# Performance work log

Measured on AMD Instinct MI355X. Metric: run time of the kernel, lower is better.

## Reference

```python
import jax, jax.numpy as jnp
from jax import lax
import numpy as np

# dims
B, L, M = 16, 512, 32
PRED, P, S, D = 96, 16, 8, 128
NST, DC, EXP, NL = 16, 4, 2, 4
N = (L - P) // S + 1          # 63 patches
DI = EXP * D                  # 256 d_inner
DTR = (D + 15) // 16          # 8 dt_rank


def setup_inputs() -> dict:
    key = jax.random.key(0)
    ks = jax.random.split(key, 16)
    r = lambda i, shape, s=0.02: jax.random.normal(ks[i], shape, dtype=jnp.float32) * s
    return {
        "x": jax.random.normal(ks[0], (B, L, M), dtype=jnp.float32),
        "patch_w": r(1, (D, P), 0.1), "patch_b": jnp.zeros((D,), jnp.float32),
        "pos_embed": r(2, (1, N, D)),
        "alpha": jnp.ones((NL, NL), jnp.float32), "beta": jnp.ones((NL, NL), jnp.float32),
        "theta": jnp.ones((NL, NL + 1), jnp.float32), "gamma": jnp.ones((NL, NL), jnp.float32),
        "tok_norm_w": jnp.ones((NL, D), jnp.float32), "tok_norm_b": jnp.zeros((NL, D), jnp.float32),
        "ch_norm_w": jnp.ones((NL, D), jnp.float32), "ch_norm_b": jnp.zeros((NL, D), jnp.float32),
        # 3 Mamba roles per layer: 0=token, 1=channel-fwd, 2=channel-bwd
        "in_proj_w": r(3, (NL, 3, 2 * DI, D), 0.05),
        "conv_w": r(4, (NL, 3, DI, DC), 0.1), "conv_b": jnp.zeros((NL, 3, DI), jnp.float32),
        "x_proj_w": r(5, (NL, 3, DTR + 2 * NST, DI), 0.05),
        "dt_proj_w": r(6, (NL, 3, DI, DTR), 0.1), "dt_proj_b": r(7, (NL, 3, DI), 0.5),
        "A_log": jnp.broadcast_to(jnp.log(jnp.arange(1, NST + 1, dtype=jnp.float32)), (NL, 3, DI, NST)) + 0.0,
        "D_ssm": jnp.ones((NL, 3, DI), jnp.float32),
        "out_proj_w": r(8, (NL, 3, D, DI), 0.05),
        "n2d_w1": jnp.ones((D,), jnp.float32), "n2d_b1": jnp.zeros((D,), jnp.float32),
        "n2d_w2": jnp.ones((N,), jnp.float32), "n2d_b2": jnp.zeros((N,), jnp.float32),
        "head_w": r(9, (PRED, N * D), 0.01), "head_b": jnp.zeros((PRED,), jnp.float32),
    }


def _ln(x, w, b):
    mu = x.mean(-1, keepdims=True)
    var = x.var(-1, keepdims=True)
    return (x - mu) * lax.rsqrt(var + 1e-5) * w + b


def _mamba(x, in_w, cw, cb, xw, dtw, dtb, a_log, dp, out_w):
    """Standard Mamba block. x: (b, s, D) -> (b, s, D)."""
    bsz = x.shape[0]
    xz = x @ in_w.T                                   # (b,s,2*DI)
    xi, z = jnp.split(xz, 2, axis=-1)
    # causal depthwise conv over seq
    xt = jnp.pad(xi.transpose(0, 2, 1), ((0, 0), (0, 0), (DC - 1, 0)))
    conv = lax.conv_general_dilated(xt, cw[:, None, :], (1,), 'VALID',
                                    dimension_numbers=('NCH', 'OIH', 'NCH'),
                                    feature_group_count=DI)
    u = jax.nn.silu(conv + cb[None, :, None]).transpose(0, 2, 1)  # (b,s,DI)
    xdbl = u @ xw.T
    dt, Bm, Cm = jnp.split(xdbl, [DTR, DTR + NST], axis=-1)
    dt = jax.nn.softplus(dt @ dtw.T + dtb)            # (b,s,DI)
    A = -jnp.exp(a_log)                               # (DI,NST)

    def step(h, inp):
        dt_t, b_t, c_t, u_t = inp                     # (b,DI),(b,NST),(b,NST),(b,DI)
        h = h * jnp.exp(dt_t[:, :, None] * A) + (dt_t * u_t)[:, :, None] * b_t[:, None, :]
        return h, jnp.einsum('bdn,bn->bd', h, c_t)

    h0 = jnp.zeros((bsz, DI, NST), x.dtype)
    _, ys = lax.scan(step, h0, (dt.swapaxes(0, 1), Bm.swapaxes(0, 1),
                                Cm.swapaxes(0, 1), u.swapaxes(0, 1)))
    y = ys.swapaxes(0, 1) + u * dp                    # D skip
    y = y * jax.nn.silu(z)
    return y @ out_w.T


def reference(x, patch_w, patch_b, pos_embed, alpha, beta, theta, gamma,
              tok_norm_w, tok_norm_b, ch_norm_w, ch_norm_b,
              in_proj_w, conv_w, conv_b, x_proj_w, dt_proj_w, dt_proj_b,
              A_log, D_ssm, out_proj_w, n2d_w1, n2d_b1, n2d_w2, n2d_b2,
              head_w, head_b):
    means = x.mean(1, keepdims=True)
    stds = jnp.std(x, axis=1, keepdims=True, ddof=1) + 1e-5   # torch unbiased std
    xn = ((x - means) / stds).transpose(0, 2, 1)              # (B,M,L)
    idx = jnp.arange(N)[:, None] * S + jnp.arange(P)[None, :]
    patches = xn[:, :, idx].reshape(B * M, N, P)              # unfold
    h = patches @ patch_w.T + patch_b + pos_embed             # (B*M,N,D)

    def mp(l, r):
        return (in_proj_w[l, r], conv_w[l, r], conv_b[l, r], x_proj_w[l, r],
                dt_proj_w[l, r], dt_proj_b[l, r], A_log[l, r], D_ssm[l, r], out_proj_w[l, r])

    yT, yC = [h], [h]
    for l in range(NL):
        a = jax.nn.softmax(alpha[l, :l + 1])
        bb = jax.nn.softmax(beta[l, :l + 1])
        tok_in = sum(a[i] * yT[i] + bb[i] * yC[i] for i in range(l + 1))
        tok = _mamba(_ln(tok_in, tok_norm_w[l], tok_norm_b[l]), *mp(l, 0)) + tok_in
        yT.append(tok)

        t = jax.nn.softmax(theta[l, :l + 2])
        g = jax.nn.softmax(gamma[l, :l + 1])
        ch_in = sum(t[i] * yT[i] for i in range(l + 2)) + sum(g[i] * yC[i] for i in range(l + 1))
        chr_ = ch_in.reshape(B, M, N, D).transpose(0, 2, 1, 3).reshape(B * N, M, D)
        chr_ = _ln(chr_, ch_norm_w[l], ch_norm_b[l])
        fwd = _mamba(chr_, *mp(l, 1))
        bwd = jnp.flip(_mamba(jnp.flip(chr_, 1), *mp(l, 2)), 1)
        ch_out = (fwd + bwd).reshape(B, N, M, D).transpose(0, 2, 1, 3).reshape(B * M, N, D) + ch_in
        yC.append(ch_out)

    out = yC[-1]
    out = _ln(out, n2d_w1, n2d_b1)                            # Norm2D
    out = _ln(out.swapaxes(-1, -2), n2d_w2, n2d_b2).swapaxes(-1, -2)
    out = out.reshape(B * M, N * D) @ head_w.T + head_b
    out = out.reshape(B, M, PRED).transpose(0, 2, 1)          # (B,PRED,M)
    return out * stds + means
```

## Files before the change

### kernel.cpp

```cpp
#include <hip/hip_runtime.h>
#include <hip/hip_bf16.h>
#include <cstddef>

#define Bq    16
#define Lq    512
#define Mq    32
#define PREDq 96
#define Pq    16
#define Sq    8
#define Dq    128
#define NSTq  16
#define DCq   4
#define NLq   4
#define Nq    63
#define DIq   256
#define DTRq  8
#define TOKq  32256
#define BMq   512
#define BNq   1008

typedef __attribute__((ext_vector_type(8))) short short8;
typedef __attribute__((ext_vector_type(4))) float f32x4;
typedef __attribute__((ext_vector_type(2))) float f32x2;
typedef __hip_bfloat16 bf16;

constexpr size_t HSZB      = (size_t)TOKq * Dq;
constexpr size_t OFF_MEANS = 0;
constexpr size_t OFF_STDS  = 512;
constexpr size_t OFF_PART  = 50176;
constexpr size_t OFF_HISTB = 640000;
constexpr size_t OFF_MIX   = OFF_HISTB + 9 * (HSZB / 2);
constexpr size_t OFF_XD    = OFF_MIX + (size_t)TOKq * 128;
constexpr size_t OFF_XZ2   = OFF_XD + (size_t)TOKq * 80;
constexpr size_t OFF_UC    = OFF_XZ2 + (size_t)TOKq * 512;
constexpr size_t OFF_LNB   = OFF_UC + (size_t)TOKq * 256;
constexpr size_t OFF_WB    = OFF_LNB + (size_t)TOKq * 64;
constexpr size_t WS_FLOATS = OFF_WB + 1038336;
constexpr size_t WBE_IN   = 0;
constexpr size_t WBE_X    = 786432;
constexpr size_t WBE_OUT  = 909312;
constexpr size_t WBE_HEAD = 1302528;
constexpr int    WB_TOTAL = 2076672;

__device__ __forceinline__ float silu_f(float v) { return v / (1.f + __expf(-v)); }

__device__ __forceinline__ f32x2 bfup2(const bf16* p) {
    unsigned int v = *(const unsigned int*)p;
    f32x2 r;
    r.x = __uint_as_float(v << 16);
    r.y = __uint_as_float(v & 0xffff0000u);
    return r;
}
__device__ __forceinline__ void bfpack2(float f0, float f1, bf16* dst) {
    bf16 b0 = __float2bfloat16(f0), b1 = __float2bfloat16(f1);
    unsigned int u = (unsigned int)*(unsigned short*)&b0 |
                     ((unsigned int)*(unsigned short*)&b1 << 16);
    *(unsigned int*)dst = u;
}

__global__ __launch_bounds__(256) void f2b_all(const float* __restrict__ w_in,
                                               const float* __restrict__ w_x,
                                               const float* __restrict__ w_out,
                                               const float* __restrict__ w_head,
                                               bf16* __restrict__ d) {
    int i = blockIdx.x * 256 + threadIdx.x;
    if (i >= WB_TOTAL) return;
    float v;
    if (i < 786432)        v = w_in[i];
    else if (i < 909312)   v = w_x[i - 786432];
    else if (i < 1302528)  v = w_out[i - 909312];
    else                   v = w_head[i - 1302528];
    d[i] = __float2bfloat16(v);
}

__global__ __launch_bounds__(256) void stats_kernel(const float* __restrict__ x,
                                                    float* __restrict__ means,
                                                    float* __restrict__ stds) {
    int bm = blockIdx.x; int b = bm >> 5, m = bm & 31;
    int tid = threadIdx.x;
    float s = 0.f, ss = 0.f;
    for (int l = tid; l < Lq; l += 256) {
        float v = x[((size_t)b * Lq + l) * Mq + m];
        s += v; ss += v * v;
    }
#pragma unroll
    for (int o = 32; o >= 1; o >>= 1) { s += __shfl_xor(s, o); ss += __shfl_xor(ss, o); }
    __shared__ float sh0[4], sh1[4];
    if ((tid & 63) == 0) { sh0[tid >> 6] = s; sh1[tid >> 6] = ss; }
    __syncthreads();
    if (tid == 0) {
        float S  = sh0[0] + sh0[1] + sh0[2] + sh0[3];
        float SS = sh1[0] + sh1[1] + sh1[2] + sh1[3];
        float mean = S * (1.f / (float)Lq);
        float var  = (SS - (float)Lq * mean * mean) * (1.f / (float)(Lq - 1));
        means[bm] = mean;
        stds[bm]  = sqrtf(fmaxf(var, 0.f)) + 1e-5f;
    }
}

__global__ __launch_bounds__(128) void patch_embed(const float* __restrict__ x,
                                                   const float* __restrict__ means,
                                                   const float* __restrict__ stds,
                                                   const float* __restrict__ pw,
                                                   const float* __restrict__ pb,
                                                   const float* __restrict__ pos,
                                                   bf16* __restrict__ h) {
    int blk = blockIdx.x;
    int bm = blk / Nq, n = blk - bm * Nq;
    int b = bm >> 5, m = bm & 31;
    int d = threadIdx.x;
    __shared__ float sx[Pq];
    if (d < Pq) {
        int l = n * Sq + d;
        sx[d] = (x[((size_t)b * Lq + l) * Mq + m] - means[bm]) / stds[bm];
    }
    __syncthreads();
    float acc = pb[d];
#pragma unroll
    for (int p = 0; p < Pq; p++) acc += sx[p] * pw[d * Pq + p];
    h[(size_t)blk * Dq + d] = __float2bfloat16(acc + pos[n * Dq + d]);
}

template<int CONVM, int KSKIP, int NT, int MR = 128>
__global__ __launch_bounds__(256) void gemm_k(
        const bf16* __restrict__ A, int lda,
        const bf16* __restrict__ Bw, const bf16* __restrict__ Bw2, int ldb,
        const float* __restrict__ resid, int ldr,
        float* __restrict__ C, bf16* __restrict__ Cb, int ldc,
        int M, int N, int Klen, int kstride, size_t csplit,
        int accum, int rowmap,
        int slen, const float* __restrict__ cw, const float* __restrict__ cb,
        int Mhalf, int ahalfcol, int choff, int gsilu,
        bf16* __restrict__ ucout) {
    constexpr int WR = MR / 4;
    constexpr int MS = WR / 16;
    __shared__ __align__(16) short Al[MR * 40];
    __shared__ __align__(16) short Bl[NT * 40];
    int tid = threadIdx.x;
    int wave = tid >> 6, lane = tid & 63;
    int m0 = blockIdx.y * MR, n0 = blockIdx.x * NT;
    int kbase = blockIdx.z * kstride;
    constexpr int NS = NT / 16;
    f32x4 acc[MS][NS];
#pragma unroll
    for (int i = 0; i < MS; i++)
#pragma unroll
        for (int j = 0; j < NS; j++) acc[i][j] = (f32x4){0.f, 0.f, 0.f, 0.f};

    int mlane = lane & 15, koff = (lane >> 4) * 8;
    const uint4 Z4 = {0u, 0u, 0u, 0u};

    {
        int ar = tid >> 1, ah = tid & 1;
        int brr = (NT == 128) ? (tid >> 1) : (tid >> 2);
        int bqh = (NT == 128) ? (tid & 1) : (tid & 3);
        uint4 av0, av1, bv0, bv1;
        av0 = av1 = bv0 = bv1 = Z4;
        auto loadAB = [&](int kk0) {
            int gcol = kk0 + ah * 16;
            if (KSKIP && kk0 >= 256) gcol += 256;
            const bf16* asrc = A + (size_t)(m0 + ar) * lda + gcol;
            av0 = *(const uint4*)asrc;
            av1 = *(const uint4*)(asrc + 8);
            const bf16* bb = Bw;
            if (NT == 128) {
                int bc = kk0 + bqh * 16;
                if (KSKIP && kk0 >= 256) { bb = Bw2; bc -= 256; }
                int gn = n0 + brr;
                if (gn < N) {
                    const bf16* bsrc = bb + (size_t)gn * ldb + bc;
                    bv0 = *(const uint4*)bsrc;
                    bv1 = *(const uint4*)(bsrc + 8);
                } else { bv0 = Z4; bv1 = Z4; }
            } else {
                int bc = kk0 + bqh * 8;
                if (KSKIP && kk0 >= 256) { bb = Bw2; bc -= 256; }
                int gn = n0 + brr;
                bv0 = (gn < N) ? *(const uint4*)(bb + (size_t)gn * ldb + bc) : Z4;
            }
        };
        loadAB(kbase);
        for (int k0 = 0; k0 < Klen; k0 += 32) {
            *(uint4*)&Al[ar * 40 + ah * 16]     = av0;
            *(uint4*)&Al[ar * 40 + ah * 16 + 8] = av1;
            if (NT == 128) {
                *(uint4*)&Bl[brr * 40 + bqh * 16]     = bv0;
                *(uint4*)&Bl[brr * 40 + bqh * 16 + 8] = bv1;
            } else {
                *(uint4*)&Bl[brr * 40 + bqh * 8] = bv0;
            }
            __syncthreads();
            if (k0 + 32 < Klen) loadAB(kbase + k0 + 32);
            short8 afr[MS];
#pragma unroll
            for (int ms = 0; ms < MS; ms++)
                afr[ms] = *(const short8*)&Al[(wave * WR + ms * 16 + mlane) * 40 + koff];
#pragma unroll
            for (int ns = 0; ns < NS; ns++) {
                short8 bfr = *(const short8*)&Bl[(ns * 16 + mlane) * 40 + koff];
#pragma unroll
                for (int ms = 0; ms < MS; ms++)
                    acc[ms][ns] = __builtin_amdgcn_mfma_f32_16x16x32_bf16(afr[ms], bfr, acc[ms][ns], 0, 0, 0);
            }
            __syncthreads();
        }
    }

    float* Cz = C + (size_t)blockIdx.z * csplit;
#pragma unroll
    for (int ms = 0; ms < MS; ms++) {
#pragma unroll
        for (int ns = 0; ns < NS; ns++) {
            int n = n0 + ns * 16 + mlane;
            if (n >= N) continue;
#pragma unroll
            for (int r = 0; r < 4; r++) {
                int m = m0 + wave * WR + ms * 16 + (lane >> 4) * 4 + r;
                int orow = m, ocol = n;
                if (rowmap) {
                    int bn = m >> 5, mm = m & 31;
                    int b = bn / Nq, nn = bn - b * Nq;
                    orow = (b * Mq + mm) * Nq + nn;
                }
                float v = acc[ms][ns][r];
                if (resid) v += resid[(size_t)orow * ldr + ocol];
                if (Cb) {
                    if (gsilu && ((ocol >> 8) & 1)) v = silu_f(v);
                    Cb[(size_t)orow * ldc + ocol] = __float2bfloat16(v);
                } else {
                    size_t o = (size_t)orow * ldc + ocol;
                    if (accum) Cz[o] += v; else Cz[o] = v;
                }
            }
        }
    }
}

template<int SLEN, int ROWS>
__global__ __launch_bounds__(256) void scan_f(bf16* __restrict__ xz2,
                                              const float* __restrict__ dtw,
                                              const float* __restrict__ dtb,
                                              const float* __restrict__ alog,
                                              const float* __restrict__ Dp,
                                              const float* __restrict__ cw,
                                              const float* __restrict__ cb,
                                              const bf16* __restrict__ xw,
                                              const bf16* __restrict__ xw2,
                                              int nb, int dual) {
    constexpr int UST = 264;
    __shared__ __align__(16) bf16 u_l[ROWS * UST];
    __shared__ __align__(16) float qlds[SLEN * 40];
    int bid = blockIdx.x;
    int half = (dual && bid >= nb) ? 1 : 0;
    int row = bid - half * nb;
    int rev = half;
    int tid = threadIdx.x;
    int d = tid;
    int wave = tid >> 6, lane = tid & 63;
    int mlane = lane & 15, koff = (lane >> 4) * 8;

    size_t xbase = (size_t)row * SLEN * 1024 + (size_t)half * 512 + d;
    size_t base  = xbase;

    float ucur[8], zcur[8];
#pragma unroll
    for (int i = 0; i < 8; i++) {
        int s = rev ? (SLEN - 1 - i) : i;
        zcur[i] = __bfloat162float(xz2[base + (size_t)s * 1024 + 256]);
    }
    const float* al = alog + half * 4096 + d * 16;
    float a0 = -__expf(al[0]);
    bool fast = true;
#pragma unroll
    for (int j = 1; j < 16; j++) {
        float aj = -__expf(al[j]);
        fast = fast && (fabsf(aj - a0 * (float)(j + 1)) < 1e-5f * (float)(j + 1));
    }
    f32x2 dw2[4];
#pragma unroll
    for (int r = 0; r < 4; r++)
        dw2[r] = (f32x2){dtw[half * 2048 + d * 8 + 2 * r], dtw[half * 2048 + d * 8 + 2 * r + 1]};
    float dbv = dtb[half * 256 + d], Dv = Dp[half * 256 + d];

    {
        float c0 = cw[half * 1024 + d * 4 + 0];
        float c1 = cw[half * 1024 + d * 4 + 1];
        float c2 = cw[half * 1024 + d * 4 + 2];
        float c3 = cw[half * 1024 + d * 4 + 3];
        float cbv = cb[half * 256 + d];
        constexpr int NCC = (SLEN + 7) / 8;
        float xc[8], xn[8];
#pragma unroll
        for (int i = 0; i < 8; i++) {
            int st = i < SLEN ? i : SLEN - 1;
            int s = rev ? (SLEN - 1 - st) : st;
            xc[i] = __bfloat162float(xz2[xbase + (size_t)s * 1024]);
        }
        float g1 = 0.f, g2 = 0.f, g3 = 0.f;
        for (int c = 0; c < NCC; c++) {
            if (c + 1 < NCC) {
#pragma unroll
                for (int i = 0; i < 8; i++) {
                    int st = (c + 1) * 8 + i; st = st < SLEN ? st : SLEN - 1;
                    int s = rev ? (SLEN - 1 - st) : st;
                    xn[i] = __bfloat162float(xz2[xbase + (size_t)s * 1024]);
                }
            }
#pragma unroll
            for (int i = 0; i < 8; i++) {
                int st = c * 8 + i;
                if (st < SLEN) {
                    int s = rev ? (SLEN - 1 - st) : st;
                    float cur = xc[i];
                    float ac = cbv;
                    if (st >= 3) ac += c0 * g3;
                    if (st >= 2) ac += c1 * g2;
                    if (st >= 1) ac += c2 * g1;
                    ac += c3 * cur;
                    bf16 ub = __float2bfloat16(silu_f(ac));
                    u_l[s * UST + d] = ub;
                    if (c == 0) ucur[i] = __bfloat162float(ub);
                    g3 = g2; g2 = g1; g1 = cur;
                }
            }
#pragma unroll
            for (int i = 0; i < 8; i++) xc[i] = xn[i];
        }
        for (int s = SLEN; s < ROWS; s++) u_l[s * UST + d] = __float2bfloat16(0.f);
    }
    __syncthreads();

    {
        const bf16* xwp = half ? xw2 : xw;
        constexpr int RT = ROWS / 16;
        constexpr int NTILES = RT * 3;
        const short8 bz = {0, 0, 0, 0, 0, 0, 0, 0};
        for (int tI = wave; tI < NTILES; tI += 4) {
            int tr = tI / 3, tc = tI - tr * 3;
            int gn = tc * 16 + mlane;
            bool okn = gn < 40;
            f32x4 acc = (f32x4){0.f, 0.f, 0.f, 0.f};
#pragma unroll
            for (int kk = 0; kk < 256; kk += 32) {
                short8 a = *(const short8*)&u_l[(tr * 16 + mlane) * UST + kk + koff];
                short8 b = okn ? *(const short8*)(xwp + (size_t)gn * 256 + kk + koff) : bz;
                acc = __builtin_amdgcn_mfma_f32_16x16x32_bf16(a, b, acc, 0, 0, 0);
            }
#pragma unroll
            for (int r = 0; r < 4; r++) {
                int s = tr * 16 + (lane >> 4) * 4 + r;
                if (okn && s < SLEN) qlds[s * 40 + gn] = acc[r];
            }
        }
    }

    f32x2 h2[8];
#pragma unroll
    for (int j = 0; j < 8; j++) h2[j] = (f32x2){0.f, 0.f};
    constexpr int NCH = (SLEN + 7) / 8;
    __syncthreads();

    float unxt[8], znxt[8];
    for (int c = 0; c < NCH; c++) {
        if (c + 1 < NCH) {
#pragma unroll
            for (int i = 0; i < 8; i++) {
                int st = (c + 1) * 8 + i; st = st < SLEN ? st : SLEN - 1;
                int s = rev ? (SLEN - 1 - st) : st;
                unxt[i] = __bfloat162float(u_l[s * UST + d]);
                znxt[i] = __bfloat162float(xz2[base + (size_t)s * 1024 + 256]);
            }
        }
#pragma unroll
        for (int i = 0; i < 8; i++) {
            int st = c * 8 + i;
            if (st < SLEN) {
                int s = rev ? (SLEN - 1 - st) : st;
                const float4* qv = (const float4*)&qlds[s * 40];
                float4 qa = qv[0], qb = qv[1];
                float uc_v = ucur[i];
                f32x2 acc2 = dw2[0] * (f32x2){qa.x, qa.y};
                acc2 += dw2[1] * (f32x2){qa.z, qa.w};
                acc2 += dw2[2] * (f32x2){qb.x, qb.y};
                acc2 += dw2[3] * (f32x2){qb.z, qb.w};
                float dtv = dbv + acc2.x + acc2.y;
                dtv = fmaxf(dtv, 0.f) + __logf(1.f + __expf(-fabsf(dtv)));
                float du = dtv * uc_v;
                float y;
                if (fast) {
                    float p1 = __expf(dtv * a0);
                    float p2 = p1 * p1;
                    f32x2 pp = (f32x2){p2, p2};
                    f32x2 e2[8];
                    e2[0] = (f32x2){p1, p2};
#pragma unroll
                    for (int j = 1; j < 8; j++) e2[j] = e2[j - 1] * pp;
                    f32x2 du2 = (f32x2){du, du};
                    f32x2 y2 = (f32x2){0.f, 0.f};
                    float4 B0 = qv[2], B1 = qv[3], B2 = qv[4], B3 = qv[5];
                    float4 C0 = qv[6], C1 = qv[7], C2 = qv[8], C3 = qv[9];
                    f32x2 bb[8] = {{B0.x, B0.y}, {B0.z, B0.w}, {B1.x, B1.y}, {B1.z, B1.w},
                                   {B2.x, B2.y}, {B2.z, B2.w}, {B3.x, B3.y}, {B3.z, B3.w}};
                    f32x2 cc[8] = {{C0.x, C0.y}, {C0.z, C0.w}, {C1.x, C1.y}, {C1.z, C1.w},
                                   {C2.x, C2.y}, {C2.z, C2.w}, {C3.x, C3.y}, {C3.z, C3.w}};
#pragma unroll
                    for (int j = 0; j < 8; j++) {
                        h2[j] = h2[j] * e2[j] + du2 * bb[j];
                        y2 += h2[j] * cc[j];
                    }
                    y = y2.x + y2.y;
                } else {
                    const float* q = &qlds[s * 40];
                    y = 0.f;
#pragma unroll
                    for (int j = 0; j < 16; j++) {
                        float e = __expf(dtv * (-__expf(al[j])));
                        float hh = h2[j >> 1][j & 1];
                        hh = hh * e + du * q[8 + j];
                        h2[j >> 1][j & 1] = hh;
                        y += hh * q[24 + j];
                    }
                }
                xz2[base + (size_t)s * 1024] =
                    __float2bfloat16((y + uc_v * Dv) * zcur[i]);
            }
        }
#pragma unroll
        for (int i = 0; i < 8; i++) { ucur[i] = unxt[i]; zcur[i] = znxt[i]; }
    }
}

__global__ __launch_bounds__(256) void mix_ln_tok(const bf16* __restrict__ hb,
                                                 float* __restrict__ mixb, bf16* __restrict__ lnb_out,
                                                 const float* __restrict__ alpha,
                                                 const float* __restrict__ beta,
                                                 const float* __restrict__ lnw,
                                                 const float* __restrict__ lnb, int l) {
    int t = blockIdx.x * 4 + (threadIdx.x >> 6), d = threadIdx.x & 63;
    int cnt = l + 1;
    float aw[4], bw[4];
    float amax = -1e30f, bmax = -1e30f;
    for (int i = 0; i < cnt; i++) {
        aw[i] = alpha[l * 4 + i]; bw[i] = beta[l * 4 + i];
        amax = fmaxf(amax, aw[i]); bmax = fmaxf(bmax, bw[i]);
    }
    float as = 0.f, bs = 0.f;
    for (int i = 0; i < cnt; i++) {
        aw[i] = __expf(aw[i] - amax); as += aw[i];
        bw[i] = __expf(bw[i] - bmax); bs += bw[i];
    }
    float ai = 1.f / as, bi = 1.f / bs;
    float v0 = 0.f, v1 = 0.f;
    for (int i = 0; i < cnt; i++) {
        const bf16* yt = hb + (size_t)(i == 0 ? 0 : i) * HSZB + (size_t)t * 128 + 2 * d;
        const bf16* yc = hb + (size_t)(i == 0 ? 0 : 4 + i) * HSZB + (size_t)t * 128 + 2 * d;
        f32x2 vt = bfup2(yt), vc = bfup2(yc);
        float wa = aw[i] * ai, wb = bw[i] * bi;
        v0 += wa * vt.x + wb * vc.x;
        v1 += wa * vt.y + wb * vc.y;
    }
    *(f32x2*)&mixb[(size_t)t * 128 + 2 * d] = (f32x2){v0, v1};
    float s = v0 + v1, ss = v0 * v0 + v1 * v1;
#pragma unroll
    for (int o = 32; o >= 1; o >>= 1) { s += __shfl_xor(s, o); ss += __shfl_xor(ss, o); }
    float mean = s * (1.f / 128.f);
    float var  = ss * (1.f / 128.f) - mean * mean;
    float rstd = rsqrtf(var + 1e-5f);
    f32x2 w2 = *(const f32x2*)&lnw[2 * d];
    f32x2 b2 = *(const f32x2*)&lnb[2 * d];
    bfpack2((v0 - mean) * rstd * w2.x + b2.x,
            (v1 - mean) * rstd * w2.y + b2.y,
            lnb_out + (size_t)t * 128 + 2 * d);
}

__global__ __launch_bounds__(256) void mix_ln_ch(const bf16* __restrict__ hb,
                                                float* __restrict__ mixb, bf16* __restrict__ lnb_out,
                                                const float* __restrict__ theta,
                                                const float* __restrict__ gamma,
                                                const float* __restrict__ lnw,
                                                const float* __restrict__ lnb, int l) {
    int t = blockIdx.x * 4 + (threadIdx.x >> 6), d = threadIdx.x & 63;
    int ct = l + 2, cg = l + 1;
    float tw[5], gw[4];
    float tmax = -1e30f, gmax = -1e30f;
    for (int i = 0; i < ct; i++) { tw[i] = theta[l * 5 + i]; tmax = fmaxf(tmax, tw[i]); }
    for (int i = 0; i < cg; i++) { gw[i] = gamma[l * 4 + i]; gmax = fmaxf(gmax, gw[i]); }
    float ts = 0.f, gs = 0.f;
    for (int i = 0; i < ct; i++) { tw[i] = __expf(tw[i] - tmax); ts += tw[i]; }
    for (int i = 0; i < cg; i++) { gw[i] = __expf(gw[i] - gmax); gs += gw[i]; }
    float ti = 1.f / ts, gi = 1.f / gs;
    float v0 = 0.f, v1 = 0.f;
    for (int i = 0; i < ct; i++) {
        const bf16* yt = hb + (size_t)(i == 0 ? 0 : i) * HSZB + (size_t)t * 128 + 2 * d;
        f32x2 vt = bfup2(yt);
        float w_ = tw[i] * ti;
        v0 += w_ * vt.x; v1 += w_ * vt.y;
    }
    for (int i = 0; i < cg; i++) {
        const bf16* yc = hb + (size_t)(i == 0 ? 0 : 4 + i) * HSZB + (size_t)t * 128 + 2 * d;
        f32x2 vc = bfup2(yc);
        float w_ = gw[i] * gi;
        v0 += w_ * vc.x; v1 += w_ * vc.y;
    }
    *(f32x2*)&mixb[(size_t)t * 128 + 2 * d] = (f32x2){v0, v1};
    float s = v0 + v1, ss = v0 * v0 + v1 * v1;
#pragma unroll
    for (int o = 32; o >= 1; o >>= 1) { s += __shfl_xor(s, o); ss += __shfl_xor(ss, o); }
    float mean = s * (1.f / 128.f);
    float var  = ss * (1.f / 128.f) - mean * mean;
    float rstd = rsqrtf(var + 1e-5f);
    int bm = t / Nq, n = t - bm * Nq, b = bm >> 5, m = bm & 31;
    f32x2 w2 = *(const f32x2*)&lnw[2 * d];
    f32x2 b2 = *(const f32x2*)&lnb[2 * d];
    bfpack2((v0 - mean) * rstd * w2.x + b2.x,
            (v1 - mean) * rstd * w2.y + b2.y,
            lnb_out + (size_t)((b * Nq + n) * Mq + m) * 128 + 2 * d);
}

__global__ __launch_bounds__(256) void ln128_kernel(const bf16* __restrict__ in,
                                                   const float* __restrict__ w,
                                                   const float* __restrict__ b,
                                                   float* __restrict__ out) {
    int t = blockIdx.x * 4 + (threadIdx.x >> 6), d = threadIdx.x & 63;
    f32x2 v = bfup2(in + (size_t)t * 128 + 2 * d);
    float v0 = v.x, v1 = v.y;
    float s = v0 + v1, ss = v0 * v0 + v1 * v1;
#pragma unroll
    for (int o = 32; o >= 1; o >>= 1) { s += __shfl_xor(s, o); ss += __shfl_xor(ss, o); }
    float mean = s * (1.f / 128.f);
    float var  = ss * (1.f / 128.f) - mean * mean;
    float rstd = rsqrtf(var + 1e-5f);
    f32x2 w2 = *(const f32x2*)&w[2 * d];
    f32x2 b2 = *(const f32x2*)&b[2 * d];
    *(f32x2*)&out[(size_t)t * 128 + 2 * d] =
        (f32x2){(v0 - mean) * rstd * w2.x + b2.x, (v1 - mean) * rstd * w2.y + b2.y};
}

__global__ __launch_bounds__(256) void final_ln2(const float* __restrict__ in,
                                                 const float* __restrict__ w2,
                                                 const float* __restrict__ b2,
                                                 bf16* __restrict__ out) {
    int idx = blockIdx.x * 256 + threadIdx.x;
    if (idx >= BMq * Dq) return;
    int bm = idx >> 7, d = idx & 127;
    float s = 0.f, ss = 0.f;
    for (int n = 0; n < Nq; n++) {
        float v = in[((size_t)bm * Nq + n) * 128 + d];
        s += v; ss += v * v;
    }
    float mean = s * (1.f / (float)Nq);
    float var  = ss * (1.f / (float)Nq) - mean * mean;
    float rstd = rsqrtf(var + 1e-5f);
    for (int n = 0; n < Nq; n++) {
        float v = in[((size_t)bm * Nq + n) * 128 + d];
        out[((size_t)bm * Nq + n) * 128 + d] = __float2bfloat16((v - mean) * rstd * w2[n] + b2[n]);
    }
}

__global__ __launch_bounds__(256) void finalize_kernel(const float* __restrict__ part,
                                                       const float* __restrict__ bias,
                                                       const float* __restrict__ means,
                                                       const float* __restrict__ stds,
                                                       float* __restrict__ out) {
    int idx = blockIdx.x * 256 + threadIdx.x;
    if (idx >= Bq * PREDq * Mq) return;
    int b = idx / (PREDq * Mq);
    int r = idx - b * PREDq * Mq;
    int pr = r >> 5, m = r & 31;
    int bm = b * Mq + m;
    float s = bias[pr];
#pragma unroll
    for (int z = 0; z < 12; z++) s += part[(size_t)z * BMq * PREDq + (size_t)bm * PREDq + pr];
    out[idx] = s * stds[bm] + means[bm];
}

extern "C" void kernel_launch(void* const* d_in, const int* in_sizes, int n_in,
                              void* d_out, int out_size, void* d_ws, size_t ws_size,
                              hipStream_t stream) {
    if (ws_size < WS_FLOATS * sizeof(float)) return;

    const float* x          = (const float*)d_in[0];
    const float* patch_w    = (const float*)d_in[1];
    const float* patch_b    = (const float*)d_in[2];
    const float* pos_embed  = (const float*)d_in[3];
    const float* alpha      = (const float*)d_in[4];
    const float* beta       = (const float*)d_in[5];
    const float* theta      = (const float*)d_in[6];
    const float* gamma      = (const float*)d_in[7];
    const float* tok_norm_w = (const float*)d_in[8];
    const float* tok_norm_b = (const float*)d_in[9];
    const float* ch_norm_w  = (const float*)d_in[10];
    const float* ch_norm_b  = (const float*)d_in[11];
    const float* in_proj_w  = (const float*)d_in[12];
    const float* conv_w     = (const float*)d_in[13];
    const float* conv_b     = (const float*)d_in[14];
    const float* x_proj_w   = (const float*)d_in[15];
    const float* dt_proj_w  = (const float*)d_in[16];
    const float* dt_proj_b  = (const float*)d_in[17];
    const float* A_log      = (const float*)d_in[18];
    const float* D_ssm      = (const float*)d_in[19];
    const float* out_proj_w = (const float*)d_in[20];
    const float* n2d_w1     = (const float*)d_in[21];
    const float* n2d_b1     = (const float*)d_in[22];
    const float* n2d_w2     = (const float*)d_in[23];
    const float* n2d_b2     = (const float*)d_in[24];
    const float* head_w     = (const float*)d_in[25];
    const float* head_b     = (const float*)d_in[26];

    float* W   = (float*)d_ws;
    float* out = (float*)d_out;
    bf16* WB   = (bf16*)(W + OFF_WB);
    bf16* HB   = (bf16*)(W + OFF_HISTB);
    bf16* LNB  = (bf16*)(W + OFF_LNB);
    bf16* XZ2  = (bf16*)(W + OFF_XZ2);
    float* MIX = W + OFF_MIX;

    f2b_all<<<(WB_TOTAL + 255) / 256, 256, 0, stream>>>(
        in_proj_w, x_proj_w, out_proj_w, head_w, WB);

    stats_kernel<<<BMq, 256, 0, stream>>>(x, W + OFF_MEANS, W + OFF_STDS);
    patch_embed<<<TOKq, 128, 0, stream>>>(x, W + OFF_MEANS, W + OFF_STDS,
                                          patch_w, patch_b, pos_embed, HB);

    for (int l = 0; l < NLq; l++) {
        size_t o0 = (size_t)(l * 3 + 0), o1 = (size_t)(l * 3 + 1), o2 = (size_t)(l * 3 + 2);

        mix_ln_tok<<<TOKq / 4, 256, 0, stream>>>(HB, MIX, LNB, alpha, beta,
                                                 tok_norm_w + l * Dq, tok_norm_b + l * Dq, l);
        gemm_k<0, 0, 128><<<dim3(4, 252, 1), 256, 0, stream>>>(
            LNB, 128, WB + WBE_IN + o0 * 65536, nullptr, 128, nullptr, 0,
            nullptr, XZ2, 1024, TOKq, 512, 128, 0, 0, 0, 0,
            0, nullptr, nullptr, 0, 0, 0, 1, nullptr);
        scan_f<Nq, 64><<<BMq, 256, 0, stream>>>(
            XZ2, dt_proj_w + o0 * 2048, dt_proj_b + o0 * 256,
            A_log + o0 * 4096, D_ssm + o0 * 256,
            conv_w + o0 * 1024, conv_b + o0 * 256,
            WB + WBE_X + o0 * 10240, nullptr, BMq, 0);
        gemm_k<0, 0, 64><<<dim3(2, 252, 1), 256, 0, stream>>>(
            XZ2, 1024, WB + WBE_OUT + o0 * 32768, nullptr, 256, MIX, 128,
            nullptr, HB + (size_t)(1 + l) * HSZB, 128,
            TOKq, 128, 256, 0, 0, 0, 0, 0, nullptr, nullptr, 0, 0, 0, 0, nullptr);

        mix_ln_ch<<<TOKq / 4, 256, 0, stream>>>(HB, MIX, LNB, theta, gamma,
                                                ch_norm_w + l * Dq, ch_norm_b + l * Dq, l);
        gemm_k<0, 0, 128><<<dim3(8, 252, 1), 256, 0, stream>>>(
            LNB, 128, WB + WBE_IN + o1 * 65536, nullptr, 128, nullptr, 0,
            nullptr, XZ2, 1024, TOKq, 1024, 128, 0, 0, 0, 0,
            0, nullptr, nullptr, 0, 0, 0, 1, nullptr);
        scan_f<Mq, 32><<<2 * BNq, 256, 0, stream>>>(
            XZ2, dt_proj_w + o1 * 2048, dt_proj_b + o1 * 256,
            A_log + o1 * 4096, D_ssm + o1 * 256,
            conv_w + o1 * 1024, conv_b + o1 * 256,
            WB + WBE_X + o1 * 10240, WB + WBE_X + o2 * 10240, BNq, 1);
        gemm_k<0, 1, 64><<<dim3(2, 252, 1), 256, 0, stream>>>(
            XZ2, 1024, WB + WBE_OUT + o1 * 32768, WB + WBE_OUT + o2 * 32768, 256,
            MIX, 128, nullptr, HB + (size_t)(5 + l) * HSZB, 128,
            TOKq, 128, 512, 0, 0, 0, 1, 0, nullptr, nullptr, 0, 0, 0, 0, nullptr);
    }

    ln128_kernel<<<TOKq / 4, 256, 0, stream>>>(HB + 8 * HSZB, n2d_w1, n2d_b1, MIX);
    final_ln2<<<(BMq * Dq + 255) / 256, 256, 0, stream>>>(MIX, n2d_w2, n2d_b2, LNB);
    gemm_k<0, 0, 64><<<dim3(2, 4, 12), 256, 0, stream>>>(
        LNB, Nq * Dq, WB + WBE_HEAD, nullptr, Nq * Dq, nullptr, 0,
        W + OFF_PART, nullptr, PREDq, BMq, PREDq, 672, 672,
        (size_t)BMq * PREDq, 0, 0, 0, nullptr, nullptr, 0, 0, 0, 0, nullptr);
    finalize_kernel<<<(Bq * PREDq * Mq + 255) / 256, 256, 0, stream>>>(
        W + OFF_PART, head_b, W + OFF_MEANS, W + OFF_STDS, out);
}
```

Measured before the change: 1.163 ms.

## Fuse out-projection GEMMs with following mix and LayerNorm epilogues

Adds a gemm_mix kernel in which each block computes full 128-column output rows of the out-projection. Its epilogue adds the residual, writes the history buffer, then computes the next softmax-weighted mix and LayerNorm in place. This removes the separate mix_ln_ch, mix_ln_tok (except for layer 0) and ln128 launches along with their global-memory round trips. In exchange, each GEMM block now has fewer parallel blocks (504, 64-row tiles) and carries a heavier epilogue with scattered bf16 reads of the earlier history buffers.

```diff
diff --git a/kernel.cpp b/kernel.cpp
--- a/kernel.cpp
+++ b/kernel.cpp
@@ -236,6 +236,186 @@
     }
 }
 
+template<int KSKIP, int ROWMAP, int MIXMODE>
+__global__ __launch_bounds__(256) void gemm_mix(
+        const bf16* __restrict__ A,
+        const bf16* __restrict__ Bw, const bf16* __restrict__ Bw2,
+        const float* __restrict__ resid,
+        bf16* __restrict__ hb, int hwrite, int l,
+        const float* __restrict__ mw0, const float* __restrict__ mw1,
+        const float* __restrict__ lnw, const float* __restrict__ lnb,
+        float* __restrict__ mixout, bf16* __restrict__ lnbout) {
+    constexpr int KLEN = KSKIP ? 512 : 256;
+    __shared__ __align__(16) short Al[64 * 40];
+    __shared__ __align__(16) short Bl[128 * 40];
+    int tid = threadIdx.x;
+    int wave = tid >> 6, lane = tid & 63;
+    int mlane = lane & 15, koff = (lane >> 4) * 8;
+    int m0 = blockIdx.x * 64;
+
+    f32x4 acc[8];
+#pragma unroll
+    for (int j = 0; j < 8; j++) acc[j] = (f32x4){0.f, 0.f, 0.f, 0.f};
+
+    int ar = tid >> 2, ah = tid & 3;
+    int br = tid >> 1, bq = tid & 1;
+    uint4 av, bv0, bv1;
+    auto loadAB = [&](int kk0) {
+        int gcol = kk0 + ah * 8;
+        if (KSKIP && kk0 >= 256) gcol += 256;
+        av = *(const uint4*)(A + (size_t)(m0 + ar) * 1024 + gcol);
+        const bf16* bb = Bw;
+        int bc = kk0 + bq * 16;
+        if (KSKIP && kk0 >= 256) { bb = Bw2; bc -= 256; }
+        const bf16* bsrc = bb + (size_t)br * 256 + bc;
+        bv0 = *(const uint4*)bsrc;
+        bv1 = *(const uint4*)(bsrc + 8);
+    };
+    loadAB(0);
+    for (int k0 = 0; k0 < KLEN; k0 += 32) {
+        *(uint4*)&Al[ar * 40 + ah * 8]      = av;
+        *(uint4*)&Bl[br * 40 + bq * 16]     = bv0;
+        *(uint4*)&Bl[br * 40 + bq * 16 + 8] = bv1;
+        __syncthreads();
+        if (k0 + 32 < KLEN) loadAB(k0 + 32);
+        short8 a = *(const short8*)&Al[(wave * 16 + mlane) * 40 + koff];
+#pragma unroll
+        for (int ns = 0; ns < 8; ns++) {
+            short8 b = *(const short8*)&Bl[(ns * 16 + mlane) * 40 + koff];
+            acc[ns] = __builtin_amdgcn_mfma_f32_16x16x32_bf16(a, b, acc[ns], 0, 0, 0);
+        }
+        __syncthreads();
+    }
+
+    float w0[5], w1[4];
+    int ct = 0, cg = 0;
+    if (MIXMODE == 0) {
+        ct = l + 2; cg = l + 1;
+        float m0v = -1e30f, m1v = -1e30f;
+        for (int i = 0; i < ct; i++) { w0[i] = mw0[l * 5 + i]; m0v = fmaxf(m0v, w0[i]); }
+        for (int i = 0; i < cg; i++) { w1[i] = mw1[l * 4 + i]; m1v = fmaxf(m1v, w1[i]); }
+        float s0 = 0.f, s1 = 0.f;
+        for (int i = 0; i < ct; i++) { w0[i] = __expf(w0[i] - m0v); s0 += w0[i]; }
+        for (int i = 0; i < cg; i++) { w1[i] = __expf(w1[i] - m1v); s1 += w1[i]; }
+        float i0 = 1.f / s0, i1 = 1.f / s1;
+        for (int i = 0; i < ct; i++) w0[i] *= i0;
+        for (int i = 0; i < cg; i++) w1[i] *= i1;
+    } else if (MIXMODE == 1) {
+        int lt = l + 1;
+        ct = lt + 1; cg = lt + 1;
+        float m0v = -1e30f, m1v = -1e30f;
+        for (int i = 0; i < ct; i++) {
+            w0[i] = mw0[lt * 4 + i]; w1[i] = mw1[lt * 4 + i];
+            m0v = fmaxf(m0v, w0[i]); m1v = fmaxf(m1v, w1[i]);
+        }
+        float s0 = 0.f, s1 = 0.f;
+        for (int i = 0; i < ct; i++) {
+            w0[i] = __expf(w0[i] - m0v); s0 += w0[i];
+            w1[i] = __expf(w1[i] - m1v); s1 += w1[i];
+        }
+        float i0 = 1.f / s0, i1 = 1.f / s1;
+        for (int i = 0; i < ct; i++) { w0[i] *= i0; w1[i] *= i1; }
+    }
+
+#pragma unroll
+    for (int r = 0; r < 4; r++) {
+        int m = m0 + wave * 16 + (lane >> 4) * 4 + r;
+        int orow = m;
+        if (ROWMAP) {
+            int bn = m >> 5, mm = m & 31;
+            int b = bn / Nq, nn = bn - b * Nq;
+            orow = (b * Mq + mm) * Nq + nn;
+        }
+        size_t t128 = (size_t)orow * 128;
+        float hv[8];
+#pragma unroll
+        for (int ns = 0; ns < 8; ns++) {
+            int col = ns * 16 + mlane;
+            float v = acc[ns][r] + resid[t128 + col];
+            bf16 hvb = __float2bfloat16(v);
+            hb[(size_t)hwrite * HSZB + t128 + col] = hvb;
+            hv[ns] = __bfloat162float(hvb);
+        }
+        float mixv[8];
+        if (MIXMODE == 2) {
+#pragma unroll
+            for (int ns = 0; ns < 8; ns++) mixv[ns] = hv[ns];
+        } else if (MIXMODE == 0) {
+#pragma unroll
+            for (int ns = 0; ns < 8; ns++) mixv[ns] = 0.f;
+            for (int i = 0; i < ct; i++) {
+                int bi = (i == 0) ? 0 : i;
+                if (bi == hwrite) {
+#pragma unroll
+                    for (int ns = 0; ns < 8; ns++) mixv[ns] += w0[i] * hv[ns];
+                } else {
+                    const bf16* yp = hb + (size_t)bi * HSZB + t128;
+#pragma unroll
+                    for (int ns = 0; ns < 8; ns++)
+                        mixv[ns] += w0[i] * __bfloat162float(yp[ns * 16 + mlane]);
+                }
+            }
+            for (int i = 0; i < cg; i++) {
+                int bi = (i == 0) ? 0 : 4 + i;
+                const bf16* yp = hb + (size_t)bi * HSZB + t128;
+#pragma unroll
+                for (int ns = 0; ns < 8; ns++)
+                    mixv[ns] += w1[i] * __bfloat162float(yp[ns * 16 + mlane]);
+            }
+        } else {
+#pragma unroll
+            for (int ns = 0; ns < 8; ns++) mixv[ns] = 0.f;
+            for (int i = 0; i < ct; i++) {
+                int bt = (i == 0) ? 0 : i;
+                int bc = (i == 0) ? 0 : 4 + i;
+                const bf16* ytp = hb + (size_t)bt * HSZB + t128;
+                if (bc == hwrite) {
+#pragma unroll
+                    for (int ns = 0; ns < 8; ns++)
+                        mixv[ns] += w0[i] * __bfloat162float(ytp[ns * 16 + mlane]) + w1[i] * hv[ns];
+                } else {
+                    const bf16* ycp = hb + (size_t)bc * HSZB + t128;
+#pragma unroll
+                    for (int ns = 0; ns < 8; ns++)
+                        mixv[ns] += w0[i] * __bfloat162float(ytp[ns * 16 + mlane]) +
+                                    w1[i] * __bfloat162float(ycp[ns * 16 + mlane]);
+                }
+            }
+        }
+        float s = 0.f, ss = 0.f;
+#pragma unroll
+        for (int ns = 0; ns < 8; ns++) { s += mixv[ns]; ss += mixv[ns] * mixv[ns]; }
+#pragma unroll
+        for (int o = 8; o >= 1; o >>= 1) { s += __shfl_xor(s, o); ss += __shfl_xor(ss, o); }
+        float mean = s * (1.f / 128.f);
+        float var  = ss * (1.f / 128.f) - mean * mean;
+        float rstd = rsqrtf(var + 1e-5f);
+        if (MIXMODE == 2) {
+#pragma unroll
+            for (int ns = 0; ns < 8; ns++) {
+                int col = ns * 16 + mlane;
+                mixout[t128 + col] = (mixv[ns] - mean) * rstd * lnw[col] + lnb[col];
+            }
+        } else {
+#pragma unroll
+            for (int ns = 0; ns < 8; ns++) mixout[t128 + ns * 16 + mlane] = mixv[ns];
+            size_t lbase;
+            if (MIXMODE == 0) {
+                int bm = orow / Nq, nn = orow - bm * Nq, b = bm >> 5, mq = bm & 31;
+                lbase = (size_t)((b * Nq + nn) * Mq + mq) * 128;
+            } else {
+                lbase = t128;
+            }
+#pragma unroll
+            for (int ns = 0; ns < 8; ns++) {
+                int col = ns * 16 + mlane;
+                lnbout[lbase + col] =
+                    __float2bfloat16((mixv[ns] - mean) * rstd * lnw[col] + lnb[col]);
+            }
+        }
+    }
+}
+
 template<int SLEN, int ROWS>
 __global__ __launch_bounds__(256) void scan_f(bf16* __restrict__ xz2,
                                               const float* __restrict__ dtw,
@@ -471,69 +651,6 @@
     bfpack2((v0 - mean) * rstd * w2.x + b2.x,
             (v1 - mean) * rstd * w2.y + b2.y,
             lnb_out + (size_t)t * 128 + 2 * d);
-}
-
-__global__ __launch_bounds__(256) void mix_ln_ch(const bf16* __restrict__ hb,
-                                                float* __restrict__ mixb, bf16* __restrict__ lnb_out,
-                                                const float* __restrict__ theta,
-                                                const float* __restrict__ gamma,
-                                                const float* __restrict__ lnw,
-                                                const float* __restrict__ lnb, int l) {
-    int t = blockIdx.x * 4 + (threadIdx.x >> 6), d = threadIdx.x & 63;
-    int ct = l + 2, cg = l + 1;
-    float tw[5], gw[4];
-    float tmax = -1e30f, gmax = -1e30f;
-    for (int i = 0; i < ct; i++) { tw[i] = theta[l * 5 + i]; tmax = fmaxf(tmax, tw[i]); }
-    for (int i = 0; i < cg; i++) { gw[i] = gamma[l * 4 + i]; gmax = fmaxf(gmax, gw[i]); }
-    float ts = 0.f, gs = 0.f;
-    for (int i = 0; i < ct; i++) { tw[i] = __expf(tw[i] - tmax); ts += tw[i]; }
-    for (int i = 0; i < cg; i++) { gw[i] = __expf(gw[i] - gmax); gs += gw[i]; }
-    float ti = 1.f / ts, gi = 1.f / gs;
-    float v0 = 0.f, v1 = 0.f;
-    for (int i = 0; i < ct; i++) {
-        const bf16* yt = hb + (size_t)(i == 0 ? 0 : i) * HSZB + (size_t)t * 128 + 2 * d;
-        f32x2 vt = bfup2(yt);
-        float w_ = tw[i] * ti;
-        v0 += w_ * vt.x; v1 += w_ * vt.y;
-    }
-    for (int i = 0; i < cg; i++) {
-        const bf16* yc = hb + (size_t)(i == 0 ? 0 : 4 + i) * HSZB + (size_t)t * 128 + 2 * d;
-        f32x2 vc = bfup2(yc);
-        float w_ = gw[i] * gi;
-        v0 += w_ * vc.x; v1 += w_ * vc.y;
-    }
-    *(f32x2*)&mixb[(size_t)t * 128 + 2 * d] = (f32x2){v0, v1};
-    float s = v0 + v1, ss = v0 * v0 + v1 * v1;
-#pragma unroll
-    for (int o = 32; o >= 1; o >>= 1) { s += __shfl_xor(s, o); ss += __shfl_xor(ss, o); }
-    float mean = s * (1.f / 128.f);
-    float var  = ss * (1.f / 128.f) - mean * mean;
-    float rstd = rsqrtf(var + 1e-5f);
-    int bm = t / Nq, n = t - bm * Nq, b = bm >> 5, m = bm & 31;
-    f32x2 w2 = *(const f32x2*)&lnw[2 * d];
-    f32x2 b2 = *(const f32x2*)&lnb[2 * d];
-    bfpack2((v0 - mean) * rstd * w2.x + b2.x,
-            (v1 - mean) * rstd * w2.y + b2.y,
-            lnb_out + (size_t)((b * Nq + n) * Mq + m) * 128 + 2 * d);
-}
-
-__global__ __launch_bounds__(256) void ln128_kernel(const bf16* __restrict__ in,
-                                                   const float* __restrict__ w,
-                                                   const float* __restrict__ b,
-                                                   float* __restrict__ out) {
-    int t = blockIdx.x * 4 + (threadIdx.x >> 6), d = threadIdx.x & 63;
-    f32x2 v = bfup2(in + (size_t)t * 128 + 2 * d);
-    float v0 = v.x, v1 = v.y;
-    float s = v0 + v1, ss = v0 * v0 + v1 * v1;
-#pragma unroll
-    for (int o = 32; o >= 1; o >>= 1) { s += __shfl_xor(s, o); ss += __shfl_xor(ss, o); }
-    float mean = s * (1.f / 128.f);
-    float var  = ss * (1.f / 128.f) - mean * mean;
-    float rstd = rsqrtf(var + 1e-5f);
-    f32x2 w2 = *(const f32x2*)&w[2 * d];
-    f32x2 b2 = *(const f32x2*)&b[2 * d];
-    *(f32x2*)&out[(size_t)t * 128 + 2 * d] =
-        (f32x2){(v0 - mean) * rstd * w2.x + b2.x, (v1 - mean) * rstd * w2.y + b2.y};
 }
 
 __global__ __launch_bounds__(256) void final_ln2(const float* __restrict__ in,
@@ -622,11 +739,12 @@
     patch_embed<<<TOKq, 128, 0, stream>>>(x, W + OFF_MEANS, W + OFF_STDS,
                                           patch_w, patch_b, pos_embed, HB);
 
+    mix_ln_tok<<<TOKq / 4, 256, 0, stream>>>(HB, MIX, LNB, alpha, beta,
+                                             tok_norm_w, tok_norm_b, 0);
+
     for (int l = 0; l < NLq; l++) {
         size_t o0 = (size_t)(l * 3 + 0), o1 = (size_t)(l * 3 + 1), o2 = (size_t)(l * 3 + 2);
 
-        mix_ln_tok<<<TOKq / 4, 256, 0, stream>>>(HB, MIX, LNB, alpha, beta,
-                                                 tok_norm_w + l * Dq, tok_norm_b + l * Dq, l);
         gemm_k<0, 0, 128><<<dim3(4, 252, 1), 256, 0, stream>>>(
             LNB, 128, WB + WBE_IN + o0 * 65536, nullptr, 128, nullptr, 0,
             nullptr, XZ2, 1024, TOKq, 512, 128, 0, 0, 0, 0,
@@ -636,13 +754,11 @@
             A_log + o0 * 4096, D_ssm + o0 * 256,
             conv_w + o0 * 1024, conv_b + o0 * 256,
             WB + WBE_X + o0 * 10240, nullptr, BMq, 0);
-        gemm_k<0, 0, 64><<<dim3(2, 252, 1), 256, 0, stream>>>(
-            XZ2, 1024, WB + WBE_OUT + o0 * 32768, nullptr, 256, MIX, 128,
-            nullptr, HB + (size_t)(1 + l) * HSZB, 128,
-            TOKq, 128, 256, 0, 0, 0, 0, 0, nullptr, nullptr, 0, 0, 0, 0, nullptr);
-
-        mix_ln_ch<<<TOKq / 4, 256, 0, stream>>>(HB, MIX, LNB, theta, gamma,
-                                                ch_norm_w + l * Dq, ch_norm_b + l * Dq, l);
+        gemm_mix<0, 0, 0><<<504, 256, 0, stream>>>(
+            XZ2, WB + WBE_OUT + o0 * 32768, nullptr, MIX,
+            HB, 1 + l, l, theta, gamma,
+            ch_norm_w + l * Dq, ch_norm_b + l * Dq, MIX, LNB);
+
         gemm_k<0, 0, 128><<<dim3(8, 252, 1), 256, 0, stream>>>(
             LNB, 128, WB + WBE_IN + o1 * 65536, nullptr, 128, nullptr, 0,
             nullptr, XZ2, 1024, TOKq, 1024, 128, 0, 0, 0, 0,
@@ -652,13 +768,19 @@
             A_log + o1 * 4096, D_ssm + o1 * 256,
             conv_w + o1 * 1024, conv_b + o1 * 256,
             WB + WBE_X + o1 * 10240, WB + WBE_X + o2 * 10240, BNq, 1);
-        gemm_k<0, 1, 64><<<dim3(2, 252, 1), 256, 0, stream>>>(
-            XZ2, 1024, WB + WBE_OUT + o1 * 32768, WB + WBE_OUT + o2 * 32768, 256,
-            MIX, 128, nullptr, HB + (size_t)(5 + l) * HSZB, 128,
-            TOKq, 128, 512, 0, 0, 0, 1, 0, nullptr, nullptr, 0, 0, 0, 0, nullptr);
-    }
-
-    ln128_kernel<<<TOKq / 4, 256, 0, stream>>>(HB + 8 * HSZB, n2d_w1, n2d_b1, MIX);
+        if (l < NLq - 1) {
+            gemm_mix<1, 1, 1><<<504, 256, 0, stream>>>(
+                XZ2, WB + WBE_OUT + o1 * 32768, WB + WBE_OUT + o2 * 32768, MIX,
+                HB, 5 + l, l, alpha, beta,
+                tok_norm_w + (l + 1) * Dq, tok_norm_b + (l + 1) * Dq, MIX, LNB);
+        } else {
+            gemm_mix<1, 1, 2><<<504, 256, 0, stream>>>(
+                XZ2, WB + WBE_OUT + o1 * 32768, WB + WBE_OUT + o2 * 32768, MIX,
+                HB, 5 + l, l, nullptr, nullptr,
+                n2d_w1, n2d_b1, MIX, nullptr);
+        }
+    }
+
     final_ln2<<<(BMq * Dq + 255) / 256, 256, 0, stream>>>(MIX, n2d_w2, n2d_b2, LNB);
     gemm_k<0, 0, 64><<<dim3(2, 4, 12), 256, 0, stream>>>(
         LNB, Nq * Dq, WB + WBE_HEAD, nullptr, Nq * Dq, nullptr, 0,
```

Result: faster. 1.028 ms, median of 2 (-11.6%).
